# Kernel tuning notes

Measured on AMD Instinct MI355X. Metric: run time of the kernel, lower is better.

Reference implementation:

```python
import jax, jax.numpy as jnp
import numpy as np

E, H = 256, 4
DH = E // H                      # head dim 64
DHALF, N, R, K = 256, 16, 16, 5  # mamba d_inner//2, d_state, dt_rank, d_conv
B, L = 2, 2048


def _ln(x, g, b):
    m = jnp.mean(x, -1, keepdims=True)
    v = jnp.var(x, -1, keepdims=True)
    return (x - m) * jax.lax.rsqrt(v + 1e-5) * g + b


def _rotate_half(x):
    y = x.reshape(x.shape[:-1] + (-1, 2))
    return jnp.stack((-y[..., 1], y[..., 0]), -1).reshape(x.shape)


def _dwconv(x, w):  # x: (B,C,L), w: (C,1,K), depthwise 'same' conv, no bias (conv_bias//2 == 0)
    return jax.lax.conv_general_dilated(
        x, w, (1,), 'SAME', feature_group_count=x.shape[1],
        dimension_numbers=('NCH', 'OIH', 'NCH'))


def _selective_scan(x, dt, A_log, Bm, Cm, Dp, dt_bias):
    # x, dt: (B,Dh,L); Bm, Cm: (B,N,L); A_log: (Dh,N); Dp, dt_bias: (Dh,)
    A = -jnp.exp(A_log)
    delta = jax.nn.softplus(dt + dt_bias[None, :, None])
    seq = (jnp.moveaxis(delta, 2, 0), jnp.moveaxis(x, 2, 0),
           jnp.moveaxis(Bm, 2, 0), jnp.moveaxis(Cm, 2, 0))
    h0 = jnp.zeros((x.shape[0], A.shape[0], A.shape[1]), x.dtype)

    def step(h, inp):
        d_l, x_l, B_l, C_l = inp
        h = jnp.exp(d_l[:, :, None] * A) * h + (d_l * x_l)[:, :, None] * B_l[:, None, :]
        return h, jnp.einsum('bdn,bn->bd', h, C_l)

    _, ys = jax.lax.scan(step, h0, seq)
    return jnp.moveaxis(ys, 0, 2) + Dp[None, :, None] * x


def _forward(desc0, desc1, pe0, pe1, qkv_w, qkv_b, attn_out_w, attn_out_b,
             ma_ffn_w1, ma_ffn_b1, ma_ffn_g, ma_ffn_beta, ma_ffn_w2, ma_ffn_b2,
             m_in_w, m_convx_w, m_convz_w, m_xproj_w, m_dt_w, m_dt_b, m_Alog, m_D, m_out_w,
             ca_qk_w, ca_qk_b, ca_v_w, ca_v_b, ca_out_w, ca_out_b,
             ca_ffn_w1, ca_ffn_b1, ca_ffn_g, ca_ffn_beta, ca_ffn_w2, ca_ffn_b2):

    def mamba_twopath(x_in):
        xz = jnp.swapaxes(x_in @ m_in_w.T, 1, 2)           # (B, 2*Dh, L)
        xc, zc = xz[:, :DHALF], xz[:, DHALF:]
        xc = jax.nn.silu(_dwconv(xc, m_convx_w))
        zc = jax.nn.silu(_dwconv(zc, m_convz_w))
        x_dbl = jnp.einsum('bdl,kd->bkl', xc, m_xproj_w)   # (B, R+2N, L)
        # dt_proj applies its bias here AND the same bias is re-added inside the scan
        # (delta_bias), exactly as in the torch source.
        dt = jnp.einsum('brl,dr->bdl', x_dbl[:, :R], m_dt_w) + m_dt_b[None, :, None]
        Bm, Cm = x_dbl[:, R:R + N], x_dbl[:, R + N:]
        y = _selective_scan(xc, dt, m_Alog, Bm, Cm, m_D, m_dt_b)  # (B, Dh, L)
        return jnp.swapaxes(y, 1, 2) @ m_out_w.T, jnp.swapaxes(zc, 1, 2) @ m_out_w.T

    def ma_ffn(h):
        h = _ln(h @ ma_ffn_w1.T + ma_ffn_b1, ma_ffn_g, ma_ffn_beta)
        return jax.nn.gelu(h, approximate=False) @ ma_ffn_w2.T + ma_ffn_b2

    def mamba_attention(x, pe):
        b, l, _ = x.shape
        qkv = (x @ qkv_w.T + qkv_b).reshape(b, l, H, DH, 3)
        qkv = jnp.swapaxes(qkv, 1, 2)                       # (B,H,L,DH,3)
        q, k, v = qkv[..., 0], qkv[..., 1], qkv[..., 2]
        q = q * pe[0] + _rotate_half(q) * pe[1]
        k = k * pe[0] + _rotate_half(k) * pe[1]
        attn = jax.nn.softmax(jnp.einsum('bhid,bhjd->bhij', q, k) * DH ** -0.5, -1)
        o = jnp.einsum('bhij,bhjd->bhid', attn, v)
        o = jnp.swapaxes(o, 1, 2).reshape(b, l, E) @ attn_out_w.T + attn_out_b
        s_x, c_x = mamba_twopath(x)
        return x + ma_ffn(jnp.concatenate([x, o, s_x, c_x], -1))

    def ca_ffn(h):
        h = _ln(h @ ca_ffn_w1.T + ca_ffn_b1, ca_ffn_g, ca_ffn_beta)
        return jax.nn.gelu(h, approximate=False) @ ca_ffn_w2.T + ca_ffn_b2

    def split_heads(t):
        b, l, _ = t.shape
        return jnp.swapaxes(t.reshape(b, l, H, DH), 1, 2)

    def cross_attn(x0, x1):
        s = DH ** -0.25  # scale**0.5 applied to both qk0 and qk1
        qk0 = split_heads(x0 @ ca_qk_w.T + ca_qk_b) * s
        qk1 = split_heads(x1 @ ca_qk_w.T + ca_qk_b) * s
        v0 = split_heads(x0 @ ca_v_w.T + ca_v_b)
        v1 = split_heads(x1 @ ca_v_w.T + ca_v_b)
        sim = jnp.einsum('bhid,bhjd->bhij', qk0, qk1)       # (B,H,L0,L1)
        m0 = jnp.einsum('bhij,bhjd->bhid', jax.nn.softmax(sim, -1), v1)
        m1 = jnp.einsum('bhji,bhjd->bhid', jax.nn.softmax(sim, -2), v0)
        b, l = x0.shape[0], x0.shape[1]
        m0 = jnp.swapaxes(m0, 1, 2).reshape(b, l, E) @ ca_out_w.T + ca_out_b
        m1 = jnp.swapaxes(m1, 1, 2).reshape(b, x1.shape[1], E) @ ca_out_w.T + ca_out_b
        x0 = x0 + ca_ffn(jnp.concatenate([x0, m0], -1))
        x1 = x1 + ca_ffn(jnp.concatenate([x1, m1], -1))
        return x0, x1

    d0 = mamba_attention(desc0, pe0)
    d1 = mamba_attention(desc1, pe1)
    return cross_attn(d0, d1)


def setup_inputs():
    key = jax.random.key(0)
    ks = jax.random.split(key, 32)
    rn = lambda i, shape, s=0.02: jax.random.normal(ks[i], shape, jnp.float32) * s
    rng = np.random.default_rng(0)
    dt = np.exp(rng.uniform(size=DHALF) * (np.log(0.1) - np.log(0.001)) + np.log(0.001))
    inv_dt = dt + np.log(-np.expm1(-dt))
    return {
        'desc0': jax.random.normal(ks[0], (B, L, E), jnp.float32),
        'desc1': jax.random.normal(ks[1], (B, L, E), jnp.float32),
        'pe0': jax.random.normal(ks[2], (2, B, 1, L, DH), jnp.float32),
        'pe1': jax.random.normal(ks[3], (2, B, 1, L, DH), jnp.float32),
        'qkv_w': rn(4, (3 * E, E)), 'qkv_b': rn(5, (3 * E,)),
        'attn_out_w': rn(6, (E, E)), 'attn_out_b': rn(7, (E,)),
        'ma_ffn_w1': rn(8, (2 * E, 4 * E)), 'ma_ffn_b1': rn(9, (2 * E,)),
        'ma_ffn_g': jnp.ones((2 * E,), jnp.float32), 'ma_ffn_beta': jnp.zeros((2 * E,), jnp.float32),
        'ma_ffn_w2': rn(10, (E, 2 * E)), 'ma_ffn_b2': rn(11, (E,)),
        'm_in_w': rn(12, (2 * DHALF, E)),
        'm_convx_w': rn(13, (DHALF, 1, K), 0.2), 'm_convz_w': rn(14, (DHALF, 1, K), 0.2),
        'm_xproj_w': rn(15, (R + 2 * N, DHALF)),
        'm_dt_w': rn(16, (DHALF, R), R ** -0.5),
        'm_dt_b': jnp.asarray(inv_dt, jnp.float32),
        'm_Alog': jnp.log(jnp.broadcast_to(jnp.arange(1, N + 1, dtype=jnp.float32), (DHALF, N))),
        'm_D': jnp.ones((DHALF,), jnp.float32),
        'm_out_w': rn(17, (E, DHALF)),
        'ca_qk_w': rn(18, (E, E)), 'ca_qk_b': rn(19, (E,)),
        'ca_v_w': rn(20, (E, E)), 'ca_v_b': rn(21, (E,)),
        'ca_out_w': rn(22, (E, E)), 'ca_out_b': rn(23, (E,)),
        'ca_ffn_w1': rn(24, (2 * E, 2 * E)), 'ca_ffn_b1': rn(25, (2 * E,)),
        'ca_ffn_g': jnp.ones((2 * E,), jnp.float32), 'ca_ffn_beta': jnp.zeros((2 * E,), jnp.float32),
        'ca_ffn_w2': rn(26, (E, 2 * E)), 'ca_ffn_b2': rn(27, (E,)),
    }


def reference(desc0, desc1, pe0, pe1, qkv_w, qkv_b, attn_out_w, attn_out_b,
              ma_ffn_w1, ma_ffn_b1, ma_ffn_g, ma_ffn_beta, ma_ffn_w2, ma_ffn_b2,
              m_in_w, m_convx_w, m_convz_w, m_xproj_w, m_dt_w, m_dt_b, m_Alog, m_D, m_out_w,
              ca_qk_w, ca_qk_b, ca_v_w, ca_v_b, ca_out_w, ca_out_b,
              ca_ffn_w1, ca_ffn_b1, ca_ffn_g, ca_ffn_beta, ca_ffn_w2, ca_ffn_b2):
    return _forward(desc0, desc1, pe0, pe1, qkv_w, qkv_b, attn_out_w, attn_out_b,
                    ma_ffn_w1, ma_ffn_b1, ma_ffn_g, ma_ffn_beta, ma_ffn_w2, ma_ffn_b2,
                    m_in_w, m_convx_w, m_convz_w, m_xproj_w, m_dt_w, m_dt_b, m_Alog, m_D, m_out_w,
                    ca_qk_w, ca_qk_b, ca_v_w, ca_v_b, ca_out_w, ca_out_b,
                    ca_ffn_w1, ca_ffn_b1, ca_ffn_g, ca_ffn_beta, ca_ffn_w2, ca_ffn_b2)
```

## Files before the change

kernel.cpp:

```cpp
#include <hip/hip_runtime.h>

typedef unsigned short u16;
typedef short s16;
typedef s16 s16x8 __attribute__((ext_vector_type(8)));
typedef float f32x4 __attribute__((ext_vector_type(4)));

__device__ __forceinline__ float bf2f(u16 u){
  union { unsigned int i; float f; } v; v.i = ((unsigned int)u) << 16; return v.f;
}
__device__ __forceinline__ u16 f2bf(float f){
  union { float f; unsigned int u; } v; v.f = f;
  unsigned int r = (v.u + 0x7fffu + ((v.u >> 16) & 1u)) >> 16;
  return (u16)r;
}
__device__ __forceinline__ unsigned int cvtpk(float lo, float hi){
  unsigned int d;
  asm("v_cvt_pk_bf16_f32 %0, %1, %2" : "=v"(d) : "v"(lo), "v"(hi));
  return d;
}
__device__ __forceinline__ uint4 pack8(float4 a0, float4 a1){
  uint4 v;
  v.x = cvtpk(a0.x, a0.y); v.y = cvtpk(a0.z, a0.w);
  v.z = cvtpk(a1.x, a1.y); v.w = cvtpk(a1.z, a1.w);
  return v;
}
__device__ __forceinline__ float gelu_f(float x){
  return 0.5f * x * (1.f + erff(x * 0.70710678118654752440f));
}
__device__ __forceinline__ float ldw(const void* p, long i, int fl){
  return fl ? bf2f(((const u16*)p)[i]) : ((const float*)p)[i];
}
__device__ __forceinline__ float4 ldw4(const void* p, long i, int fl){
  if (fl){
    ushort4 w = *(const ushort4*)((const u16*)p + i);
    return make_float4(bf2f(w.x), bf2f(w.y), bf2f(w.z), bf2f(w.w));
  }
  return *(const float4*)((const float*)p + i);
}

template<int C>
__device__ __forceinline__ float dppf(float x){
  return __int_as_float(__builtin_amdgcn_update_dpp(0, __float_as_int(x), C, 0xf, 0xf, true));
}
__device__ __forceinline__ float dppmax16(float v){
  v = fmaxf(v, dppf<0xB1>(v));
  v = fmaxf(v, dppf<0x4E>(v));
  v = fmaxf(v, dppf<0x141>(v));
  v = fmaxf(v, dppf<0x140>(v));
  return v;
}
__device__ __forceinline__ float dppsum16(float v){
  v += dppf<0xB1>(v);
  v += dppf<0x4E>(v);
  v += dppf<0x141>(v);
  v += dppf<0x140>(v);
  return v;
}

__global__ __launch_bounds__(256) void k_sniff(const unsigned int* __restrict__ w,
                                               int n, int* __restrict__ flag){
  __shared__ int cnt[256];
  int c = 0;
  for (int i = threadIdx.x; i < n; i += 256){
    unsigned e = (w[i] >> 7) & 0xFFu;
    c += (e >= 120u && e <= 127u) ? 1 : 0;
  }
  cnt[threadIdx.x] = c; __syncthreads();
  for (int s = 128; s > 0; s >>= 1){
    if (threadIdx.x < s) cnt[threadIdx.x] += cnt[threadIdx.x + s];
    __syncthreads();
  }
  if (threadIdx.x == 0) flag[0] = (2 * cnt[0] > n) ? 1 : 0;
  if (threadIdx.x == 1) flag[1] = 0;
  if (threadIdx.x == 2) flag[2] = 1;
}

struct WC { const void* src[13]; int off[14]; };
__global__ __launch_bounds__(256) void k_wconv(WC wc, u16* __restrict__ dst,
                                               const int* __restrict__ flagp){
  int fl = *flagp;
  int i = blockIdx.x * 256 + threadIdx.x;
  if (i >= wc.off[13]) return;
  int s = 0;
  #pragma unroll
  for (int t = 1; t < 13; ++t) s += (i >= wc.off[t]) ? 1 : 0;
  dst[i] = f2bf(ldw(wc.src[s], i - wc.off[s], fl));
}

__global__ __launch_bounds__(256) void k_pad(
  const void* __restrict__ wx, const void* __restrict__ wd,
  const void* __restrict__ bd,
  u16* __restrict__ px, u16* __restrict__ pd, float* __restrict__ pb,
  const int* __restrict__ flagp)
{
  int fl = *flagp;
  int i = blockIdx.x * 256 + threadIdx.x;
  if (i < 16384){
    int r = i >> 8, c = i & 255;
    px[i] = f2bf((r < 48) ? ldw(wx, r*256 + c, fl) : 0.f);
  } else if (i < 32768){
    int j = i - 16384;
    int n = j >> 6, k = j & 63;
    pd[j] = f2bf((k < 16) ? ldw(wd, n*16 + k, fl) : 0.f);
  } else if (i < 33024){
    pb[i - 32768] = ldw(bd, i - 32768, fl);
  }
}

__global__ __launch_bounds__(256) void k_gemm_mfma(
  const void* __restrict__ A0, int aflidx, int lda, int K, int N,
  const u16* __restrict__ W, const u16* __restrict__ W2, int nsplit, int wflidx,
  const void* __restrict__ bias,
  float* __restrict__ Cf0, u16* __restrict__ Cb, int ldc,
  float* __restrict__ C20, int ldc2,
  const void* __restrict__ resid, int rflidx, int ldr,
  float oscale, int act_gelu, int outmode,
  const void* __restrict__ A1, long coff1, long c2off1,
  const int* __restrict__ flagp)
{
  const int fl  = flagp[0];
  const int afl = flagp[aflidx];
  const int wfl = flagp[wflidx];
  const int rfl = flagp[rflidx];
  const void* A = A0;
  float* Cf = Cf0;
  float* C2 = C20;
  if (blockIdx.z){ A = A1; Cf += coff1; C2 += c2off1; }
  __shared__ u16 As[64*72];
  __shared__ u16 Bs[64*72];
  const int tid = threadIdx.x;
  const int w = tid >> 6, lane = tid & 63, quad = lane >> 4, m = lane & 15;
  const int m0 = blockIdx.y << 6, n0 = blockIdx.x << 6;
  const int srow = tid >> 2, sc0 = (tid & 3) << 4;
  const int reg2 = (n0 >= nsplit);
  const u16* Wp = reg2 ? W2 : W;
  const int nbase = reg2 ? nsplit : 0;

  f32x4 acc[4];
  #pragma unroll
  for (int ct = 0; ct < 4; ++ct) acc[ct] = (f32x4){0.f,0.f,0.f,0.f};

  for (int k0 = 0; k0 < K; k0 += 64){
    {
      long ab = (long)(m0 + srow) * lda + k0 + sc0;
      if (afl && !act_gelu){
        #pragma unroll
        for (int g = 0; g < 2; ++g)
          *(uint4*)&As[srow*72 + sc0 + g*8] = *(const uint4*)((const u16*)A + ab + g*8);
      } else {
        #pragma unroll
        for (int g = 0; g < 2; ++g){
          float4 a0 = ldw4(A, ab + g*8, afl);
          float4 a1 = ldw4(A, ab + g*8 + 4, afl);
          if (act_gelu){
            a0.x=gelu_f(a0.x); a0.y=gelu_f(a0.y); a0.z=gelu_f(a0.z); a0.w=gelu_f(a0.w);
            a1.x=gelu_f(a1.x); a1.y=gelu_f(a1.y); a1.z=gelu_f(a1.z); a1.w=gelu_f(a1.w);
          }
          *(uint4*)&As[srow*72 + sc0 + g*8] = pack8(a0, a1);
        }
      }
    }
    {
      long wb = (long)(n0 + srow - nbase) * K + k0 + sc0;
      #pragma unroll
      for (int g = 0; g < 2; ++g)
        *(uint4*)&Bs[srow*72 + sc0 + g*8] = *(const uint4*)(Wp + wb + g*8);
    }
    __syncthreads();

    s16x8 av[2];
    #pragma unroll
    for (int s = 0; s < 2; ++s)
      av[s] = *(const s16x8*)&As[(w*16 + m)*72 + s*32 + quad*8];
    #pragma unroll
    for (int ct = 0; ct < 4; ++ct)
      #pragma unroll
      for (int s = 0; s < 2; ++s){
        s16x8 bv = *(const s16x8*)&Bs[(ct*16 + m)*72 + s*32 + quad*8];
        acc[ct] = __builtin_amdgcn_mfma_f32_16x16x32_bf16(av[s], bv, acc[ct], 0, 0, 0);
      }
    __syncthreads();
  }

  if (outmode == 4){
    const int gmb = m0 + w*16 + quad*4;
    #pragma unroll
    for (int ct = 0; ct < 4; ++ct){
      int gn = n0 + ct*16 + m;
      float bv = ldw(bias, gn, wfl);
      float dl4[4], dx4[4];
      #pragma unroll
      for (int r = 0; r < 4; ++r){
        float dl = acc[ct][r] + bv + bv;
        float delta = (dl > 20.f) ? dl : __logf(1.f + __expf(dl));
        dl4[r] = delta;
        dx4[r] = delta * ldw(resid, (long)(gmb + r) * ldr + gn, rfl);
      }
      *(float4*)&Cf[(long)gn * ldc + gmb] = make_float4(dl4[0], dl4[1], dl4[2], dl4[3]);
      *(float4*)&C2[(long)gn * ldc2 + gmb] = make_float4(dx4[0], dx4[1], dx4[2], dx4[3]);
    }
    return;
  }

  #pragma unroll
  for (int r = 0; r < 4; ++r){
    int gm = m0 + w*16 + quad*4 + r;
    #pragma unroll
    for (int ct = 0; ct < 4; ++ct){
      int gn = n0 + ct*16 + m;
      float v = acc[ct][r];
      if (reg2){
        C2[(long)gm * ldc2 + (gn - nsplit)] = v;
      } else {
        if (bias) v += ldw(bias, gn, wfl);
        v *= oscale;
        if (resid) v += ldw(resid, (long)gm * ldr + gn, rfl);
        long off = (long)gm * ldc + gn;
        if (outmode == 2){
          if (fl) Cb[off] = f2bf(v); else Cf[off] = v;
        } else if (outmode == 3){
          Cb[off] = f2bf(v);
        } else {
          Cf[off] = v;
        }
      }
    }
  }
}

struct GB8 {
  const void* A[8]; const u16* W[8]; const void* bias[8];
  float* Cf[8]; u16* Cb[8]; const void* resid[8];
  const void* csrc[8]; u16* cdst[8]; float osc[8];
  int cfl[8]; int wkoff[8]; int rfli[8]; int afli[8];
  const float* aux[8]; const void* dvec;
};

__global__ __launch_bounds__(256) void k_gemmb(
  GB8 gb, int lda, int K, int N, int ldc, int ldr, int ldwq,
  int act_gelu, int outmode, const int* __restrict__ flagp)
{
  const int fl = flagp[0];
  const int z = blockIdx.z;
  const void* A = gb.A[z]; const u16* W = gb.W[z]; const void* bias = gb.bias[z];
  float* Cf = gb.Cf[z]; u16* Cb = gb.Cb[z]; const void* resid = gb.resid[z];
  const void* csrc = gb.csrc[z]; u16* cdst = gb.cdst[z];
  const float osc = gb.osc[z];
  const int cfl = flagp[gb.cfl[z]];
  const int rfl = flagp[gb.rfli[z]];
  const int wkoff = gb.wkoff[z];
  const int abf = gb.afli[z];
  const float* aux = gb.aux[z];

  __shared__ u16 As[64*72];
  __shared__ u16 Bs[64*72];
  const int tid = threadIdx.x;
  const int w = tid >> 6, lane = tid & 63, quad = lane >> 4, m = lane & 15;
  const int m0 = blockIdx.y << 6, n0 = blockIdx.x << 6;
  const int srow = tid >> 2, sc0 = (tid & 3) << 4;

  f32x4 acc[4];
  #pragma unroll
  for (int ct = 0; ct < 4; ++ct) acc[ct] = (f32x4){0.f,0.f,0.f,0.f};

  for (int k0 = 0; k0 < K; k0 += 64){
    if (abf){
      const u16* ar = (const u16*)A + (long)(m0 + srow) * lda + k0 + sc0;
      #pragma unroll
      for (int g = 0; g < 2; ++g)
        *(uint4*)&As[srow*72 + sc0 + g*8] = *(const uint4*)(ar + g*8);
    } else {
      const float* ar = (const float*)A + (long)(m0 + srow) * lda + k0 + sc0;
      #pragma unroll
      for (int g = 0; g < 2; ++g){
        float4 a0 = *(const float4*)(ar + g*8);
        float4 a1 = *(const float4*)(ar + g*8 + 4);
        if (aux){
          const float* xr = aux + (long)(m0 + srow) * lda + k0 + sc0;
          float4 x0 = *(const float4*)(xr + g*8);
          float4 x1 = *(const float4*)(xr + g*8 + 4);
          float4 d0 = ldw4(gb.dvec, k0 + sc0 + g*8, fl);
          float4 d1 = ldw4(gb.dvec, k0 + sc0 + g*8 + 4, fl);
          a0.x += d0.x*x0.x; a0.y += d0.y*x0.y; a0.z += d0.z*x0.z; a0.w += d0.w*x0.w;
          a1.x += d1.x*x1.x; a1.y += d1.y*x1.y; a1.z += d1.z*x1.z; a1.w += d1.w*x1.w;
        }
        if (act_gelu){
          a0.x=gelu_f(a0.x); a0.y=gelu_f(a0.y); a0.z=gelu_f(a0.z); a0.w=gelu_f(a0.w);
          a1.x=gelu_f(a1.x); a1.y=gelu_f(a1.y); a1.z=gelu_f(a1.z); a1.w=gelu_f(a1.w);
        }
        *(uint4*)&As[srow*72 + sc0 + g*8] = pack8(a0, a1);
      }
    }
    {
      long wb = (long)(n0 + srow) * ldwq + wkoff + k0 + sc0;
      #pragma unroll
      for (int g = 0; g < 2; ++g)
        *(uint4*)&Bs[srow*72 + sc0 + g*8] = *(const uint4*)(W + wb + g*8);
    }
    __syncthreads();

    s16x8 av[2];
    #pragma unroll
    for (int s = 0; s < 2; ++s)
      av[s] = *(const s16x8*)&As[(w*16 + m)*72 + s*32 + quad*8];
    #pragma unroll
    for (int ct = 0; ct < 4; ++ct)
      #pragma unroll
      for (int s = 0; s < 2; ++s){
        s16x8 bv = *(const s16x8*)&Bs[(ct*16 + m)*72 + s*32 + quad*8];
        acc[ct] = __builtin_amdgcn_mfma_f32_16x16x32_bf16(av[s], bv, acc[ct], 0, 0, 0);
      }
    __syncthreads();
  }

  #pragma unroll
  for (int r = 0; r < 4; ++r){
    int gm = m0 + w*16 + quad*4 + r;
    #pragma unroll
    for (int ct = 0; ct < 4; ++ct){
      int gn = n0 + ct*16 + m;
      float v = acc[ct][r];
      if (bias) v += ldw(bias, gn, fl);
      v *= osc;
      if (resid) v += ldw(resid, (long)gm * ldr + gn, rfl);
      long off = (long)gm * ldc + gn;
      if (outmode == 2){
        if (fl) Cb[off] = f2bf(v); else Cf[off] = v;
      } else if (outmode == 3){
        Cb[off] = f2bf(v);
      } else if (outmode == 5){
        Cf[off] = v; Cb[off] = f2bf(v);
      } else {
        Cf[off] = v;
      }
      if (cdst) cdst[(long)gm * ldc + gn] = f2bf(ldw(csrc, (long)gm * 256 + gn, cfl));
    }
  }
}

__global__ __launch_bounds__(256) void k_rope(
  const float* __restrict__ qkv0, const float* __restrict__ qkv1,
  const void* __restrict__ pe0, const void* __restrict__ pe1,
  u16* __restrict__ q, u16* __restrict__ k, u16* __restrict__ v,
  int L, int B, int H, const int* __restrict__ flagp)
{
  int fl = *flagp;
  int tid = threadIdx.x;
  int lq = tid >> 6, d = tid & 63;
  int l = blockIdx.x * 4 + lq;
  int bh = blockIdx.y;
  int dsc = bh >> 3;
  int bh7 = bh & 7;
  int b = bh7 >> 2, h = bh7 & 3;
  const float* qkv = dsc ? qkv1 : qkv0;
  const void* pe = dsc ? pe1 : pe0;
  const float* row = qkv + ((long)b * L + l) * 768 + h * 192;
  float qv = row[d*3+0], kv = row[d*3+1], vv = row[d*3+2];
  int dn = (d & 1) ? (d - 1) : (d + 1);
  float qn = row[dn*3+0], kn = row[dn*3+1];
  float rq = (d & 1) ? qn : -qn;
  float rk = (d & 1) ? kn : -kn;
  long peo = ((long)b * L + l) * 64 + d;
  float p0 = ldw(pe, peo, fl);
  float p1 = ldw(pe, (long)B * L * 64 + peo, fl);
  long o = ((long)bh * L + l) * 64 + d;
  q[o] = f2bf((qv * p0 + rq * p1) * 0.18033688011112042f);
  k[o] = f2bf(kv * p0 + rk * p1);
  v[o] = f2bf(vv);
}

__global__ __launch_bounds__(256, 8) void k_attn_mfma(
  const u16* __restrict__ Q, long qsb, long qsh, long qsl,
  const u16* __restrict__ Kp, long ksb, long ksh, long ksl,
  const u16* __restrict__ Vp, long vsb, long vsh, long vsl,
  float* __restrict__ Opart, float* __restrict__ mpart, float* __restrict__ lpart,
  int L, int H, int kchunk, int bxor)
{
  __shared__ u16 Kt[64*72];
  __shared__ u16 Vt[64*72];
  __shared__ u16 Ps[64*72];
  const int tid  = threadIdx.x;
  const int w    = tid >> 6;
  const int lane = tid & 63;
  const int quad = lane >> 4;
  const int m    = lane & 15;

  int bx = blockIdx.x, by = blockIdx.y, bz = blockIdx.z;
  if (gridDim.x == 32 && gridDim.y == 16 && gridDim.z == 2){
    int lid = bx + (by << 5) + (bz << 9);
    int xcd = lid & 7, slot = lid >> 3;
    int combo = xcd * 4 + (slot >> 5);
    bx = slot & 31; by = combo & 15; bz = combo >> 4;
  }
  const int bh = by, b = bh / H, h = bh % H;
  const int iq0 = bx * 64;
  const int z = bz;
  const long BHL = (long)gridDim.y * L;

  const u16* Qb = Q  + (long)b*qsb + h*qsh;
  const u16* Kb = Kp + (long)(b^bxor)*ksb + h*ksh;
  const u16* Vb = Vp + (long)(b^bxor)*vsb + h*vsh;

  s16x8 aq[2];
  {
    const u16* qr = Qb + (long)(iq0 + w*16 + m) * qsl + quad*8;
    aq[0] = *(const s16x8*)(qr);
    aq[1] = *(const s16x8*)(qr + 32);
  }

  f32x4 o_acc[4];
  #pragma unroll
  for (int nt = 0; nt < 4; ++nt) o_acc[nt] = (f32x4){0.f,0.f,0.f,0.f};
  float mrow[4] = {-1e30f,-1e30f,-1e30f,-1e30f};
  float lsum[4] = {0.f,0.f,0.f,0.f};

  const int srow = tid >> 2, sc0 = (tid & 3) << 4;
  const int kg = tid & 15;
  const int dg = tid >> 4;
  const int vcb = ((((dg >> 2) * 2) + (kg >> 1)) & 7) * 8 + (kg & 1) * 4;
  const int modd = m & 1;
  const int pcolb = m & 6;
  const int jend = z * kchunk + kchunk;

  for (int j0 = z * kchunk; j0 < jend; j0 += 64){
    {
      const u16* kr = Kb + (long)(j0 + srow) * ksl + sc0;
      *(uint4*)&Kt[srow*72 + sc0]     = *(const uint4*)kr;
      *(uint4*)&Kt[srow*72 + sc0 + 8] = *(const uint4*)(kr + 8);
      const u16* vr = Vb + (long)(j0 + 4*kg) * vsl + 4*dg;
      ushort4 r0 = *(const ushort4*)(vr);
      ushort4 r1 = *(const ushort4*)(vr + vsl);
      ushort4 r2 = *(const ushort4*)(vr + 2*vsl);
      ushort4 r3 = *(const ushort4*)(vr + 3*vsl);
      u16* vt = &Vt[(4*dg)*72 + vcb];
      *(ushort4*)(vt)       = make_ushort4(r0.x, r1.x, r2.x, r3.x);
      *(ushort4*)(vt + 72)  = make_ushort4(r0.y, r1.y, r2.y, r3.y);
      *(ushort4*)(vt + 144) = make_ushort4(r0.z, r1.z, r2.z, r3.z);
      *(ushort4*)(vt + 216) = make_ushort4(r0.w, r1.w, r2.w, r3.w);
    }
    __syncthreads();

    float sv[4][4];
    #pragma unroll
    for (int ct = 0; ct < 4; ++ct){
      f32x4 acc = (f32x4){0.f,0.f,0.f,0.f};
      #pragma unroll
      for (int s = 0; s < 2; ++s){
        s16x8 bk = *(const s16x8*)&Kt[(ct*16 + m)*72 + s*32 + quad*8];
        acc = __builtin_amdgcn_mfma_f32_16x16x32_bf16(aq[s], bk, acc, 0, 0, 0);
      }
      #pragma unroll
      for (int r = 0; r < 4; ++r) sv[ct][r] = acc[r];
    }

    float v0[4];
    int need = 0;
    #pragma unroll
    for (int r = 0; r < 4; ++r){
      v0[r] = fmaxf(fmaxf(sv[0][r], sv[1][r]), fmaxf(sv[2][r], sv[3][r]));
      need |= (v0[r] > mrow[r] + 8.f) ? 1 : 0;
    }
    if (__any(need)){
      float alpha[4];
      #pragma unroll
      for (int r = 0; r < 4; ++r){
        float mx = dppmax16(v0[r]);
        float mn = fmaxf(mrow[r], mx);
        alpha[r] = exp2f(mrow[r] - mn);
        mrow[r] = mn;
        lsum[r] *= alpha[r];
      }
      #pragma unroll
      for (int nt = 0; nt < 4; ++nt)
        #pragma unroll
        for (int r = 0; r < 4; ++r) o_acc[nt][r] *= alpha[r];
    }
    #pragma unroll
    for (int ct = 0; ct < 4; ++ct)
      #pragma unroll
      for (int r = 0; r < 4; ++r){
        float p = exp2f(sv[ct][r] - mrow[r]);
        sv[ct][r] = p;
        lsum[r] += p;
      }

    #pragma unroll
    for (int ct = 0; ct < 4; ++ct){
      const int kb = (2*w + 2*ct + (m >> 3)) & 7;
      const int col = (kb << 3) | pcolb;
      #pragma unroll
      for (int rr = 0; rr < 2; ++rr){
        float nb_lo = dppf<0xB1>(sv[ct][rr]);
        float nb_hi = dppf<0xB1>(sv[ct][2+rr]);
        float lo = modd ? nb_hi       : sv[ct][rr];
        float hi = modd ? sv[ct][2+rr] : nb_lo;
        unsigned int pk = cvtpk(lo, hi);
        int row = w*16 + quad*4 + rr + 2*modd;
        *(unsigned int*)&Ps[row*72 + col] = pk;
      }
    }
    asm volatile("s_waitcnt lgkmcnt(0)" ::: "memory");

    s16x8 ap[2];
    #pragma unroll
    for (int s = 0; s < 2; ++s)
      ap[s] = *(const s16x8*)&Ps[(w*16 + m)*72 + (((2*w + 4*s + quad) & 7) << 3)];
    #pragma unroll
    for (int nt = 0; nt < 4; ++nt)
      #pragma unroll
      for (int s = 0; s < 2; ++s){
        s16x8 bv = *(const s16x8*)&Vt[(nt*16 + m)*72 + (((2*nt + 4*s + quad) & 7) << 3)];
        o_acc[nt] = __builtin_amdgcn_mfma_f32_16x16x32_bf16(ap[s], bv, o_acc[nt], 0, 0, 0);
      }
    __syncthreads();
  }

  const long zOoff = (long)z * BHL * 64;
  #pragma unroll
  for (int r = 0; r < 4; ++r){
    int iq = iq0 + w*16 + quad*4 + r;
    long rowid = ((long)b*L + iq) * H + h;
    #pragma unroll
    for (int nt = 0; nt < 4; ++nt)
      Opart[zOoff + rowid*64 + nt*16 + m] = o_acc[nt][r];
    float lr = dppsum16(lsum[r]);
    if (m == 0){
      mpart[(long)z*BHL + rowid] = mrow[r];
      lpart[(long)z*BHL + rowid] = lr;
    }
  }
}

__global__ __launch_bounds__(256) void k_attn_comb(
  const float* Opart, const float* mpart, const float* lpart,
  u16* O, long BHL, int nz)
{
  long i = (long)blockIdx.x * 256 + threadIdx.x;
  long row = i >> 6;
  float mv[4];
  float M = -1e30f;
  for (int z = 0; z < nz; ++z){
    mv[z] = mpart[(long)z*BHL + row];
    M = fmaxf(M, mv[z]);
  }
  long N64 = BHL * 64;
  float T = 0.f, acc = 0.f;
  for (int z = 0; z < nz; ++z){
    float wz = exp2f(mv[z] - M);
    T   += lpart[(long)z*BHL + row] * wz;
    acc += Opart[(long)z*N64 + i] * wz;
  }
  O[i] = f2bf(acc / T);
}

__global__ __launch_bounds__(256) void k_conv2(
  const float* __restrict__ xz,
  const void* __restrict__ wx, const void* __restrict__ wz,
  float* __restrict__ outxf, u16* __restrict__ outxb, u16* __restrict__ outzb,
  int L, const int* __restrict__ flagp)
{
  int fl = *flagp;
  int c = threadIdx.x;
  int bl = blockIdx.x; int b = bl / L, l = bl % L;
  int choff = blockIdx.y ? 256 : 0;
  const void* w = blockIdx.y ? wz : wx;
  const float* base = xz + ((long)b * L) * 512 + choff + c;
  float s = 0.f;
  #pragma unroll
  for (int kk = 0; kk < 5; ++kk){
    int ll = l + kk - 2;
    if (ll >= 0 && ll < L) s += base[(long)ll * 512] * ldw(w, c*5 + kk, fl);
  }
  s = s / (1.f + __expf(-s));
  long idx = ((long)b * L + l) * 256 + c;
  if (blockIdx.y){
    outzb[idx] = f2bf(s);
  } else {
    outxf[idx] = s;
    outxb[idx] = f2bf(s);
  }
}

#define SC_CS 64
#define SC_NC 32

__global__ __launch_bounds__(256) void k_scan1(
  const float* __restrict__ deltaT, const float* __restrict__ dxcT,
  const float* __restrict__ xdbl, const void* __restrict__ Alog,
  float* __restrict__ E_out, float* __restrict__ F_out,
  int L, int ldt, const int* __restrict__ flagp)
{
  int fl = *flagp;
  int tid = threadIdx.x;
  int g = tid >> 4, n = tid & 15;
  int gid = blockIdx.x * 16 + g;
  int chunk = gid & (SC_NC - 1);
  int p = gid >> 5;
  int b = p >> 8, d = p & 255;
  float A = -__expf(ldw(Alog, d*16 + n, fl));
  const float* dTp = deltaT + (long)d*ldt + (long)b*L;
  const float* dxp = dxcT  + (long)d*ldt + (long)b*L;
  const float* xdb = xdbl + (long)b*L*64;
  int l0 = chunk * SC_CS;
  float E = 1.f, F = 0.f;
  for (int i = 0; i < SC_CS; i += 4){
    int l = l0 + i;
    float4 dt4 = *(const float4*)(dTp + l);
    float4 dx4 = *(const float4*)(dxp + l);
    float e[4], u[4];
    e[0] = __expf(dt4.x * A); e[1] = __expf(dt4.y * A);
    e[2] = __expf(dt4.z * A); e[3] = __expf(dt4.w * A);
    u[0] = dx4.x * xdb[(l+0)*64 + 16 + n];
    u[1] = dx4.y * xdb[(l+1)*64 + 16 + n];
    u[2] = dx4.z * xdb[(l+2)*64 + 16 + n];
    u[3] = dx4.w * xdb[(l+3)*64 + 16 + n];
    F = e[0]*F + u[0]; F = e[1]*F + u[1];
    F = e[2]*F + u[2]; F = e[3]*F + u[3];
    E *= (e[0]*e[1]) * (e[2]*e[3]);
  }
  long idx = (long)(p*16 + n) * SC_NC + chunk;
  E_out[idx] = E; F_out[idx] = F;
}

__global__ __launch_bounds__(256) void k_scan2(
  const float* __restrict__ E, const float* __restrict__ F,
  float* __restrict__ Hin)
{
  int pn = blockIdx.x * 256 + threadIdx.x;
  const float* Ep = E + (long)pn * SC_NC;
  const float* Fp = F + (long)pn * SC_NC;
  float* Hp = Hin + (long)pn * SC_NC;
  float h = 0.f;
  #pragma unroll
  for (int c = 0; c < SC_NC; ++c){
    Hp[c] = h;
    h = Ep[c] * h + Fp[c];
  }
}

__global__ __launch_bounds__(256) void k_scan3(
  const float* __restrict__ deltaT, const float* __restrict__ dxcT,
  const float* __restrict__ xdbl, const void* __restrict__ Alog,
  const float* __restrict__ Hin, float* __restrict__ y,
  int L, int ldt, const int* __restrict__ flagp)
{
  int fl = *flagp;
  int tid = threadIdx.x;
  int g = tid >> 4, n = tid & 15;
  int gid = blockIdx.x * 16 + g;
  int chunk = gid & (SC_NC - 1);
  int p = gid >> 5;
  int b = p >> 8, d = p & 255;
  float A = -__expf(ldw(Alog, d*16 + n, fl));
  const float* dTp = deltaT + (long)d*ldt + (long)b*L;
  const float* dxp = dxcT  + (long)d*ldt + (long)b*L;
  const float* xdb = xdbl + (long)b*L*64;
  float* yb = y + (long)b*L*256 + d;
  long idx = (long)(p*16 + n) * SC_NC + chunk;
  float h = Hin[idx];
  int l0 = chunk * SC_CS;
  for (int i = 0; i < SC_CS; i += 4){
    int l = l0 + i;
    float4 dt4 = *(const float4*)(dTp + l);
    float4 dx4 = *(const float4*)(dxp + l);
    float e[4], u[4], cm[4];
    e[0] = __expf(dt4.x * A); e[1] = __expf(dt4.y * A);
    e[2] = __expf(dt4.z * A); e[3] = __expf(dt4.w * A);
    u[0] = dx4.x * xdb[(l+0)*64 + 16 + n];
    u[1] = dx4.y * xdb[(l+1)*64 + 16 + n];
    u[2] = dx4.z * xdb[(l+2)*64 + 16 + n];
    u[3] = dx4.w * xdb[(l+3)*64 + 16 + n];
    cm[0] = xdb[(l+0)*64 + 32 + n];
    cm[1] = xdb[(l+1)*64 + 32 + n];
    cm[2] = xdb[(l+2)*64 + 32 + n];
    cm[3] = xdb[(l+3)*64 + 32 + n];
    float s0, s1, s2, s3;
    h = e[0]*h + u[0]; s0 = h * cm[0];
    h = e[1]*h + u[1]; s1 = h * cm[1];
    h = e[2]*h + u[2]; s2 = h * cm[2];
    h = e[3]*h + u[3]; s3 = h * cm[3];
    s0 += __shfl_xor(s0, 1, 16); s1 += __shfl_xor(s1, 1, 16);
    s2 += __shfl_xor(s2, 1, 16); s3 += __shfl_xor(s3, 1, 16);
    s0 += __shfl_xor(s0, 2, 16); s1 += __shfl_xor(s1, 2, 16);
    s2 += __shfl_xor(s2, 2, 16); s3 += __shfl_xor(s3, 2, 16);
    s0 += __shfl_xor(s0, 4, 16); s1 += __shfl_xor(s1, 4, 16);
    s2 += __shfl_xor(s2, 4, 16); s3 += __shfl_xor(s3, 4, 16);
    s0 += __shfl_xor(s0, 8, 16); s1 += __shfl_xor(s1, 8, 16);
    s2 += __shfl_xor(s2, 8, 16); s3 += __shfl_xor(s3, 8, 16);
    if (n < 4){
      float out = (n == 0) ? s0 : (n == 1) ? s1 : (n == 2) ? s2 : s3;
      yb[(long)(l + n)*256] = out;
    }
  }
}

__global__ __launch_bounds__(256) void k_ln2(
  float* __restrict__ hA, const float* __restrict__ hA2,
  float* __restrict__ hB, const float* __restrict__ hB2,
  const void* __restrict__ g, const void* __restrict__ beta,
  const int* __restrict__ flagp)
{
  int fl = *flagp;
  int r = blockIdx.x * 4 + (threadIdx.x >> 6);
  float* hbase = (r < 4096) ? hA : hB;
  const float* h2base = (r < 4096) ? hA2 : hB2;
  int row = r & 4095;
  int lane = threadIdx.x & 63;
  float* hr = hbase + (long)row * 512;
  const float* h2r = h2base + (long)row * 512;
  float v[8]; float s = 0.f, ss = 0.f;
  #pragma unroll
  for (int i = 0; i < 8; ++i){
    v[i] = hr[lane + 64*i] + h2r[lane + 64*i];
    s += v[i]; ss += v[i]*v[i];
  }
  #pragma unroll
  for (int off = 1; off < 64; off <<= 1){ s += __shfl_xor(s, off); ss += __shfl_xor(ss, off); }
  float mean = s * (1.f/512.f);
  float var  = ss * (1.f/512.f) - mean * mean;
  float rs = rsqrtf(var + 1e-5f);
  #pragma unroll
  for (int i = 0; i < 8; ++i){
    int c = lane + 64*i;
    hr[c] = (v[i] - mean) * rs * ldw(g, c, fl) + ldw(beta, c, fl);
  }
}

extern "C" void kernel_launch(void* const* d_in, const int* in_sizes, int n_in,
                              void* d_out, int out_size, void* d_ws, size_t ws_size,
                              hipStream_t stream)
{
  const int B_ = 2, L_ = 2048, H_ = 4;
  const long BLE = (long)B_ * L_ * 256;
  const long BHLb = 2L * B_ * H_ * L_;

  int* flagp = (int*)d_ws;
  float* base = (float*)d_ws + 64;

  float* cat0   = base + 0*BLE;
  float* cat1   = base + 3*BLE;
  float* xz01   = base + 6*BLE;
  u16*   q01    = (u16*)(base + 10*BLE);
  u16*   k01    = (u16*)(base + 11*BLE);
  u16*   v01    = (u16*)(base + 12*BLE);
  float* Opart  = base + 13*BLE;
  u16*   obb    = (u16*)(base + 17*BLE);
  float* mml    = base + 18*BLE;
  float* mll    = mml + 2*32768;
  float* xc_f   = base + 19*BLE;
  u16*   xcb    = (u16*)(base + 21*BLE);
  u16*   zcb    = (u16*)(base + 22*BLE);
  float* xdbl01 = base + 23*BLE;
  float* delta01= base + 24*BLE;
  float* dxc01  = base + 26*BLE;
  float* scE    = base + 28*BLE;
  float* scF    = scE + 524288;
  float* scH    = scF + 524288;
  float* y01    = base + 30*BLE;
  u16*   catc0b = (u16*)(base + 32*BLE);
  u16*   catc1b = (u16*)(base + 34*BLE);
  float* h0     = base + 36*BLE;
  float* part0  = base + 38*BLE;
  float* h1     = base + 40*BLE;
  float* part1  = base + 42*BLE;
  float* dbuf0  = base + 44*BLE;
  float* dbuf1  = base + 45*BLE;
  u16*   dbuf0b = (u16*)(base + 46*BLE);
  u16*   dbuf1b = dbuf0b + 1048576;
  u16*   qc     = (u16*)(base + 47*BLE);
  u16*   kc     = qc + 1048576;
  u16*   vc     = kc + 1048576;
  u16*   oc     = vc + 1048576;
  u16*   cm     = (u16*)(base + 49*BLE);
  u16*   catAb  = (u16*)(base + 50*BLE);
  u16*   catBb  = (u16*)(base + 51*BLE);
  u16*   px     = (u16*)(base + 52*BLE);
  u16*   pd     = px + 16384;
  float* pb     = (float*)(pd + 16384);
  u16*   wbuf   = (u16*)(base + 53*BLE);

  const void* in[35];
  for (int i = 0; i < 35 && i < n_in; ++i) in[i] = d_in[i];

  const int woff[14] = {
    0,
    196608,
    327680,
    393216,
    917504,
    1048576,
    1114112,
    1179648,
    1245184,
    1310720,
    1572864,
    1703936,
    2752512,
    3801088 };
  const u16* wqkv  = wbuf + woff[0];
  const u16* wxz   = wbuf + woff[1];
  const u16* wattn = wbuf + woff[2];
  const u16* wffn1 = wbuf + woff[3];
  const u16* wffn2 = wbuf + woff[4];
  const u16* wout  = wbuf + woff[5];
  const u16* wcqk  = wbuf + woff[6];
  const u16* wcv   = wbuf + woff[7];
  const u16* wcout = wbuf + woff[8];
  const u16* wcf1  = wbuf + woff[9];
  const u16* wcf2  = wbuf + woff[10];
  const u16* bin0  = wbuf + woff[11];
  const u16* bin1  = wbuf + woff[12];

  k_sniff<<<1, 256, 0, stream>>>((const unsigned int*)in[0], 2048, flagp);
  {
    WC wc = {};
    wc.src[0]=in[4]; wc.src[1]=in[14]; wc.src[2]=in[6]; wc.src[3]=in[8];
    wc.src[4]=in[12]; wc.src[5]=in[22]; wc.src[6]=in[23]; wc.src[7]=in[25];
    wc.src[8]=in[27]; wc.src[9]=in[29]; wc.src[10]=in[33];
    wc.src[11]=in[0]; wc.src[12]=in[1];
    for (int t = 0; t < 14; ++t) wc.off[t] = woff[t];
    k_wconv<<<(woff[13] + 255)/256, 256, 0, stream>>>(wc, wbuf, flagp);
  }
  k_pad<<<130, 256, 0, stream>>>(in[17], in[18], in[19], px, pd, pb, flagp);

  const int BIG = 1 << 30;
  const long sbP = (long)H_ * L_ * 64, shP = (long)L_ * 64, slP = 64;
  const long sbF = (long)L_ * 256,     shF = 64,            slF = 256;
  const int NZ = 2;
  const int kchunk = L_ / NZ;
  const int MROWS = 4 * L_;
  const float LOG2E = 1.4426950408889634f;

  k_gemm_mfma<<<dim3(20, 64, 2), 256, 0, stream>>>(
      bin0, 2, 256, 256, 1280, wqkv, wxz, 768, 0, in[5],
      cat0, nullptr, 768, xz01, 512,
      nullptr, 1, 0, 1.f, 0, 0,
      bin1, 3*BLE, 2*BLE, flagp);
  k_rope<<<dim3(L_/4, 16), 256, 0, stream>>>(cat0, cat1, in[2], in[3],
      q01, k01, v01, L_, B_, H_, flagp);
  k_attn_mfma<<<dim3(L_/64, 16, NZ), 256, 0, stream>>>(
      q01, sbP, shP, slP, k01, sbP, shP, slP, v01, sbP, shP, slP,
      Opart, mml, mll, L_, H_, kchunk, 0);
  k_attn_comb<<<8192, 256, 0, stream>>>(Opart, mml, mll, obb, BHLb, NZ);
  k_conv2<<<dim3(2*B_*L_, 2), 256, 0, stream>>>(xz01, in[15], in[16], xc_f, xcb, zcb, L_, flagp);
  k_gemm_mfma<<<dim3(1, 128), 256, 0, stream>>>(
      xcb, 2, 256, 256, 64, px, nullptr, BIG, 1, nullptr,
      xdbl01, nullptr, 64, nullptr, 0,
      nullptr, 1, 0, 1.f, 0, 0,
      nullptr, 0, 0, flagp);
  k_gemm_mfma<<<dim3(4, 128), 256, 0, stream>>>(
      xdbl01, 1, 64, 64, 256, pd, nullptr, BIG, 1, pb,
      delta01, nullptr, MROWS, dxc01, MROWS,
      xc_f, 1, 256, 1.f, 0, 4,
      nullptr, 0, 0, flagp);
  k_scan1<<<2048, 256, 0, stream>>>(delta01, dxc01, xdbl01, in[20], scE, scF, L_, MROWS, flagp);
  k_scan2<<<64, 256, 0, stream>>>(scE, scF, scH);
  k_scan3<<<2048, 256, 0, stream>>>(delta01, dxc01, xdbl01, in[20], scH, y01, L_, MROWS, flagp);
  {
    GB8 gb = {};
    gb.dvec = in[21];
    gb.A[0] = y01;        gb.aux[0] = xc_f;       gb.W[0] = wout; gb.Cb[0] = catc0b + 512; gb.osc[0] = 1.f; gb.cfl[0] = 1;
    gb.A[1] = zcb;        gb.afli[1] = 1;         gb.W[1] = wout; gb.Cb[1] = catc0b + 768; gb.osc[1] = 1.f; gb.cfl[1] = 1;
    gb.A[2] = obb;        gb.afli[2] = 1;         gb.W[2] = wattn; gb.bias[2] = in[7];     gb.Cb[2] = catc0b + 256;
    gb.csrc[2] = in[0];   gb.cdst[2] = catc0b;    gb.osc[2] = 1.f; gb.cfl[2] = 0;
    gb.A[3] = y01 + BLE;  gb.aux[3] = xc_f + BLE; gb.W[3] = wout; gb.Cb[3] = catc1b + 512; gb.osc[3] = 1.f; gb.cfl[3] = 1;
    gb.A[4] = zcb + 1048576; gb.afli[4] = 1;      gb.W[4] = wout; gb.Cb[4] = catc1b + 768; gb.osc[4] = 1.f; gb.cfl[4] = 1;
    gb.A[5] = obb + 1048576; gb.afli[5] = 1;      gb.W[5] = wattn; gb.bias[5] = in[7];     gb.Cb[5] = catc1b + 256;
    gb.csrc[5] = in[1];   gb.cdst[5] = catc1b;    gb.osc[5] = 1.f; gb.cfl[5] = 0;
    k_gemmb<<<dim3(4, 64, 6), 256, 0, stream>>>(gb, 256, 256, 256, 1024, 0, 256, 0, 3, flagp);
  }
  {
    GB8 gb = {};
    gb.cfl[0] = gb.cfl[1] = gb.cfl[2] = gb.cfl[3] = 1;
    gb.afli[0] = gb.afli[1] = gb.afli[2] = gb.afli[3] = 1;
    gb.A[0] = catc0b;       gb.W[0] = wffn1; gb.bias[0] = in[9]; gb.Cf[0] = h0;    gb.osc[0] = 1.f;
    gb.A[1] = catc0b + 512; gb.W[1] = wffn1; gb.wkoff[1] = 512;  gb.Cf[1] = part0; gb.osc[1] = 1.f;
    gb.A[2] = catc1b;       gb.W[2] = wffn1; gb.bias[2] = in[9]; gb.Cf[2] = h1;    gb.osc[2] = 1.f;
    gb.A[3] = catc1b + 512; gb.W[3] = wffn1; gb.wkoff[3] = 512;  gb.Cf[3] = part1; gb.osc[3] = 1.f;
    k_gemmb<<<dim3(8, 64, 4), 256, 0, stream>>>(gb, 1024, 512, 512, 512, 0, 1024, 0, 0, flagp);
  }
  k_ln2<<<2048, 256, 0, stream>>>(h0, part0, h1, part1, in[10], in[11], flagp);
  {
    GB8 gb = {};
    gb.cfl[0] = gb.cfl[1] = 1;
    gb.A[0] = h0; gb.W[0] = wffn2; gb.bias[0] = in[13]; gb.resid[0] = in[0]; gb.rfli[0] = 0;
    gb.Cf[0] = dbuf0; gb.Cb[0] = dbuf0b; gb.osc[0] = 1.f;
    gb.A[1] = h1; gb.W[1] = wffn2; gb.bias[1] = in[13]; gb.resid[1] = in[1]; gb.rfli[1] = 0;
    gb.Cf[1] = dbuf1; gb.Cb[1] = dbuf1b; gb.osc[1] = 1.f;
    k_gemmb<<<dim3(4, 64, 2), 256, 0, stream>>>(gb, 512, 512, 256, 256, 256, 512, 1, 5, flagp);
  }

  const float s4 = 0.35355339059327373f;
  {
    GB8 gb = {};
    gb.cfl[0] = gb.cfl[1] = gb.cfl[2] = gb.cfl[3] = 1;
    gb.afli[0] = gb.afli[1] = gb.afli[2] = gb.afli[3] = 1;
    gb.A[0] = dbuf0b; gb.W[0] = wcqk; gb.bias[0] = in[24]; gb.Cb[0] = qc; gb.osc[0] = s4 * LOG2E;
    gb.A[1] = dbuf1b; gb.W[1] = wcqk; gb.bias[1] = in[24]; gb.Cb[1] = kc; gb.osc[1] = s4;
    gb.A[2] = dbuf0b; gb.W[2] = wcv;  gb.bias[2] = in[26]; gb.Cb[2] = vc; gb.osc[2] = 1.f;
    gb.A[3] = dbuf1b; gb.W[3] = wcv;  gb.bias[3] = in[26]; gb.Cb[3] = oc; gb.osc[3] = 1.f;
    k_gemmb<<<dim3(4, 64, 4), 256, 0, stream>>>(gb, 256, 256, 256, 256, 0, 256, 0, 3, flagp);
  }
  k_attn_mfma<<<dim3(L_/64, 16, NZ), 256, 0, stream>>>(
      qc, sbF, shF, slF, qc, sbF, shF, slF, vc, sbF, shF, slF,
      Opart, mml, mll, L_, H_, kchunk, 2);
  k_attn_comb<<<8192, 256, 0, stream>>>(Opart, mml, mll, cm, BHLb, NZ);
  {
    GB8 gb = {};
    gb.cfl[0] = gb.cfl[1] = 1;
    gb.afli[0] = gb.afli[1] = 1;
    gb.A[0] = cm;           gb.W[0] = wcout; gb.bias[0] = in[28]; gb.Cb[0] = catAb + 256;
    gb.csrc[0] = dbuf0;     gb.cdst[0] = catAb; gb.osc[0] = 1.f;
    gb.A[1] = cm + 1048576; gb.W[1] = wcout; gb.bias[1] = in[28]; gb.Cb[1] = catBb + 256;
    gb.csrc[1] = dbuf1;     gb.cdst[1] = catBb; gb.osc[1] = 1.f;
    k_gemmb<<<dim3(4, 64, 2), 256, 0, stream>>>(gb, 256, 256, 256, 512, 0, 256, 0, 3, flagp);
  }
  {
    GB8 gb = {};
    gb.cfl[0] = gb.cfl[1] = gb.cfl[2] = gb.cfl[3] = 1;
    gb.afli[0] = gb.afli[1] = gb.afli[2] = gb.afli[3] = 1;
    gb.A[0] = catAb;       gb.W[0] = wcf1; gb.bias[0] = in[30]; gb.Cf[0] = h0;    gb.osc[0] = 1.f;
    gb.A[1] = catAb + 256; gb.W[1] = wcf1; gb.wkoff[1] = 256;   gb.Cf[1] = part0; gb.osc[1] = 1.f;
    gb.A[2] = catBb;       gb.W[2] = wcf1; gb.bias[2] = in[30]; gb.Cf[2] = h1;    gb.osc[2] = 1.f;
    gb.A[3] = catBb + 256; gb.W[3] = wcf1; gb.wkoff[3] = 256;   gb.Cf[3] = part1; gb.osc[3] = 1.f;
    k_gemmb<<<dim3(8, 64, 4), 256, 0, stream>>>(gb, 512, 256, 512, 512, 0, 512, 0, 0, flagp);
  }
  k_ln2<<<2048, 256, 0, stream>>>(h0, part0, h1, part1, in[31], in[32], flagp);
  {
    GB8 gb = {};
    gb.cfl[0] = gb.cfl[1] = 1;
    gb.rfli[0] = gb.rfli[1] = 1;
    gb.A[0] = h0; gb.W[0] = wcf2; gb.bias[0] = in[34]; gb.resid[0] = dbuf0;
    gb.Cf[0] = (float*)d_out; gb.Cb[0] = (u16*)d_out; gb.osc[0] = 1.f;
    gb.A[1] = h1; gb.W[1] = wcf2; gb.bias[1] = in[34]; gb.resid[1] = dbuf1;
    gb.Cf[1] = (float*)d_out + BLE; gb.Cb[1] = (u16*)d_out + BLE; gb.osc[1] = 1.f;
    k_gemmb<<<dim3(4, 64, 2), 256, 0, stream>>>(gb, 512, 512, 256, 256, 256, 512, 1, 2, flagp);
  }
}
```

Measured before the change: 588.3 us.

## Store V transposed at producers so attention loads V fragments directly

```diff
diff --git a/kernel.cpp b/kernel.cpp
--- a/kernel.cpp
+++ b/kernel.cpp
@@ -232,7 +232,7 @@
   const void* A[8]; const u16* W[8]; const void* bias[8];
   float* Cf[8]; u16* Cb[8]; const void* resid[8];
   const void* csrc[8]; u16* cdst[8]; float osc[8];
-  int cfl[8]; int wkoff[8]; int rfli[8]; int afli[8];
+  int cfl[8]; int wkoff[8]; int rfli[8]; int afli[8]; int vtr[8];
   const float* aux[8]; const void* dvec;
 };
 
@@ -313,6 +313,24 @@
     __syncthreads();
   }
 
+  if (gb.vtr[z]){
+    const int gmb = m0 + w*16 + quad*4;
+    const int b2 = gmb >> 11;
+    const int l  = gmb & 2047;
+    #pragma unroll
+    for (int ct = 0; ct < 4; ++ct){
+      int gn = n0 + ct*16 + m;
+      float bb = bias ? ldw(bias, gn, fl) : 0.f;
+      ushort4 o4;
+      o4.x = f2bf((acc[ct][0] + bb) * osc);
+      o4.y = f2bf((acc[ct][1] + bb) * osc);
+      o4.z = f2bf((acc[ct][2] + bb) * osc);
+      o4.w = f2bf((acc[ct][3] + bb) * osc);
+      *(ushort4*)&Cb[((long)(b2*256 + gn)) * 2048 + l] = o4;
+    }
+    return;
+  }
+
   #pragma unroll
   for (int r = 0; r < 4; ++r){
     int gm = m0 + w*16 + quad*4 + r;
@@ -341,9 +359,10 @@
 __global__ __launch_bounds__(256) void k_rope(
   const float* __restrict__ qkv0, const float* __restrict__ qkv1,
   const void* __restrict__ pe0, const void* __restrict__ pe1,
-  u16* __restrict__ q, u16* __restrict__ k, u16* __restrict__ v,
+  u16* __restrict__ q, u16* __restrict__ k, u16* __restrict__ vT,
   int L, int B, int H, const int* __restrict__ flagp)
 {
+  __shared__ u16 vt[4][64];
   int fl = *flagp;
   int tid = threadIdx.x;
   int lq = tid >> 6, d = tid & 63;
@@ -366,7 +385,12 @@
   long o = ((long)bh * L + l) * 64 + d;
   q[o] = f2bf((qv * p0 + rq * p1) * 0.18033688011112042f);
   k[o] = f2bf(kv * p0 + rk * p1);
-  v[o] = f2bf(vv);
+  vt[lq][d] = f2bf(vv);
+  __syncthreads();
+  if (tid < 64){
+    ushort4 o4 = make_ushort4(vt[0][tid], vt[1][tid], vt[2][tid], vt[3][tid]);
+    *(ushort4*)&vT[((long)bh*64 + tid)*L + blockIdx.x*4] = o4;
+  }
 }
 
 __global__ __launch_bounds__(256, 8) void k_attn_mfma(
@@ -377,7 +401,6 @@
   int L, int H, int kchunk, int bxor)
 {
   __shared__ u16 Kt[64*72];
-  __shared__ u16 Vt[64*72];
   __shared__ u16 Ps[64*72];
   const int tid  = threadIdx.x;
   const int w    = tid >> 6;
@@ -415,28 +438,21 @@
   float lsum[4] = {0.f,0.f,0.f,0.f};
 
   const int srow = tid >> 2, sc0 = (tid & 3) << 4;
-  const int kg = tid & 15;
-  const int dg = tid >> 4;
-  const int vcb = ((((dg >> 2) * 2) + (kg >> 1)) & 7) * 8 + (kg & 1) * 4;
   const int modd = m & 1;
   const int pcolb = m & 6;
   const int jend = z * kchunk + kchunk;
 
   for (int j0 = z * kchunk; j0 < jend; j0 += 64){
+    s16x8 bvv[4][2];
+    #pragma unroll
+    for (int nt = 0; nt < 4; ++nt)
+      #pragma unroll
+      for (int s = 0; s < 2; ++s)
+        bvv[nt][s] = *(const s16x8*)(Vb + (long)(nt*16 + m)*vsl + j0 + s*32 + quad*8);
     {
       const u16* kr = Kb + (long)(j0 + srow) * ksl + sc0;
       *(uint4*)&Kt[srow*72 + sc0]     = *(const uint4*)kr;
       *(uint4*)&Kt[srow*72 + sc0 + 8] = *(const uint4*)(kr + 8);
-      const u16* vr = Vb + (long)(j0 + 4*kg) * vsl + 4*dg;
-      ushort4 r0 = *(const ushort4*)(vr);
-      ushort4 r1 = *(const ushort4*)(vr + vsl);
-      ushort4 r2 = *(const ushort4*)(vr + 2*vsl);
-      ushort4 r3 = *(const ushort4*)(vr + 3*vsl);
-      u16* vt = &Vt[(4*dg)*72 + vcb];
-      *(ushort4*)(vt)       = make_ushort4(r0.x, r1.x, r2.x, r3.x);
-      *(ushort4*)(vt + 72)  = make_ushort4(r0.y, r1.y, r2.y, r3.y);
-      *(ushort4*)(vt + 144) = make_ushort4(r0.z, r1.z, r2.z, r3.z);
-      *(ushort4*)(vt + 216) = make_ushort4(r0.w, r1.w, r2.w, r3.w);
     }
     __syncthreads();
 
@@ -508,10 +524,8 @@
     #pragma unroll
     for (int nt = 0; nt < 4; ++nt)
       #pragma unroll
-      for (int s = 0; s < 2; ++s){
-        s16x8 bv = *(const s16x8*)&Vt[(nt*16 + m)*72 + (((2*nt + 4*s + quad) & 7) << 3)];
-        o_acc[nt] = __builtin_amdgcn_mfma_f32_16x16x32_bf16(ap[s], bv, o_acc[nt], 0, 0, 0);
-      }
+      for (int s = 0; s < 2; ++s)
+        o_acc[nt] = __builtin_amdgcn_mfma_f32_16x16x32_bf16(ap[s], bvv[nt][s], o_acc[nt], 0, 0, 0);
     __syncthreads();
   }
 
@@ -742,7 +756,7 @@
   float* xz01   = base + 6*BLE;
   u16*   q01    = (u16*)(base + 10*BLE);
   u16*   k01    = (u16*)(base + 11*BLE);
-  u16*   v01    = (u16*)(base + 12*BLE);
+  u16*   vT01   = (u16*)(base + 12*BLE);
   float* Opart  = base + 13*BLE;
   u16*   obb    = (u16*)(base + 17*BLE);
   float* mml    = base + 18*BLE;
@@ -769,8 +783,7 @@
   u16*   dbuf1b = dbuf0b + 1048576;
   u16*   qc     = (u16*)(base + 47*BLE);
   u16*   kc     = qc + 1048576;
-  u16*   vc     = kc + 1048576;
-  u16*   oc     = vc + 1048576;
+  u16*   vcT    = kc + 1048576;
   u16*   cm     = (u16*)(base + 49*BLE);
   u16*   catAb  = (u16*)(base + 50*BLE);
   u16*   catBb  = (u16*)(base + 51*BLE);
@@ -826,6 +839,7 @@
   const int BIG = 1 << 30;
   const long sbP = (long)H_ * L_ * 64, shP = (long)L_ * 64, slP = 64;
   const long sbF = (long)L_ * 256,     shF = 64,            slF = 256;
+  const long vsb = 256L * L_, vsh = 64L * L_, vsl = L_;
   const int NZ = 2;
   const int kchunk = L_ / NZ;
   const int MROWS = 4 * L_;
@@ -837,9 +851,9 @@
       nullptr, 1, 0, 1.f, 0, 0,
       bin1, 3*BLE, 2*BLE, flagp);
   k_rope<<<dim3(L_/4, 16), 256, 0, stream>>>(cat0, cat1, in[2], in[3],
-      q01, k01, v01, L_, B_, H_, flagp);
+      q01, k01, vT01, L_, B_, H_, flagp);
   k_attn_mfma<<<dim3(L_/64, 16, NZ), 256, 0, stream>>>(
-      q01, sbP, shP, slP, k01, sbP, shP, slP, v01, sbP, shP, slP,
+      q01, sbP, shP, slP, k01, sbP, shP, slP, vT01, vsb, vsh, vsl,
       Opart, mml, mll, L_, H_, kchunk, 0);
   k_attn_comb<<<8192, 256, 0, stream>>>(Opart, mml, mll, obb, BHLb, NZ);
   k_conv2<<<dim3(2*B_*L_, 2), 256, 0, stream>>>(xz01, in[15], in[16], xc_f, xcb, zcb, L_, flagp);
@@ -895,14 +909,15 @@
     GB8 gb = {};
     gb.cfl[0] = gb.cfl[1] = gb.cfl[2] = gb.cfl[3] = 1;
     gb.afli[0] = gb.afli[1] = gb.afli[2] = gb.afli[3] = 1;
+    gb.vtr[2] = gb.vtr[3] = 1;
     gb.A[0] = dbuf0b; gb.W[0] = wcqk; gb.bias[0] = in[24]; gb.Cb[0] = qc; gb.osc[0] = s4 * LOG2E;
     gb.A[1] = dbuf1b; gb.W[1] = wcqk; gb.bias[1] = in[24]; gb.Cb[1] = kc; gb.osc[1] = s4;
-    gb.A[2] = dbuf0b; gb.W[2] = wcv;  gb.bias[2] = in[26]; gb.Cb[2] = vc; gb.osc[2] = 1.f;
-    gb.A[3] = dbuf1b; gb.W[3] = wcv;  gb.bias[3] = in[26]; gb.Cb[3] = oc; gb.osc[3] = 1.f;
+    gb.A[2] = dbuf0b; gb.W[2] = wcv;  gb.bias[2] = in[26]; gb.Cb[2] = vcT; gb.osc[2] = 1.f;
+    gb.A[3] = dbuf1b; gb.W[3] = wcv;  gb.bias[3] = in[26]; gb.Cb[3] = vcT + 1048576; gb.osc[3] = 1.f;
     k_gemmb<<<dim3(4, 64, 4), 256, 0, stream>>>(gb, 256, 256, 256, 256, 0, 256, 0, 3, flagp);
   }
   k_attn_mfma<<<dim3(L_/64, 16, NZ), 256, 0, stream>>>(
-      qc, sbF, shF, slF, qc, sbF, shF, slF, vc, sbF, shF, slF,
+      qc, sbF, shF, slF, qc, sbF, shF, slF, vcT, vsb, vsh, vsl,
       Opart, mml, mll, L_, H_, kchunk, 2);
   k_attn_comb<<<8192, 256, 0, stream>>>(Opart, mml, mll, cm, BHLb, NZ);
   {
```

Result: slower. 848.1 us (+44.2%).
